# Optimization experiments

Hardware: AMD Instinct MI355X
Metric: run time of the kernel (lower is better)

The kernel has to match this reference:

```python
import jax, jax.numpy as jnp
import numpy as np

N, E = 50000, 800000
IN_DIM, HID, HEADS, OUT_DIM = 128, 64, 4, 64
NEG_SLOPE = 0.2


def add_self_loops(edge_index, n):
    loops = jnp.arange(n, dtype=edge_index.dtype)
    return jnp.concatenate([edge_index, jnp.stack([loops, loops])], axis=1)


def gat_layer(x, edge_index, W, att_src, att_dst, bias, heads, ch, concat):
    n = x.shape[0]
    xp = (x @ W).reshape(n, heads, ch)                       # [N,H,C]
    s_src = jnp.sum(xp * att_src, axis=-1)                   # [N,H]
    s_dst = jnp.sum(xp * att_dst, axis=-1)                   # [N,H]
    src, dst = edge_index[0], edge_index[1]
    e = jax.nn.leaky_relu(s_src[src] + s_dst[dst], NEG_SLOPE)  # [E,H]
    # segment softmax over incoming edges of each destination node
    m = jax.ops.segment_max(e, dst, num_segments=n)
    e = jnp.exp(e - m[dst])
    denom = jax.ops.segment_sum(e, dst, num_segments=n)
    alpha = e / (denom[dst] + 1e-16)                         # [E,H]
    out = jax.ops.segment_sum(xp[src] * alpha[:, :, None], dst, num_segments=n)  # [N,H,C]
    out = out.reshape(n, heads * ch) if concat else out.mean(axis=1)
    return out + bias


def setup_inputs() -> dict:
    key = jax.random.key(0)
    ks = jax.random.split(key, 10)
    glorot = lambda k, shape: jax.random.normal(k, shape, jnp.float32) * np.sqrt(2.0 / (shape[0] + shape[-1]))
    return {
        "x": jax.random.normal(ks[0], (N, IN_DIM), jnp.float32),
        "edge_index": jax.random.randint(ks[1], (2, E), 0, N, jnp.int32),
        "W1": glorot(ks[2], (IN_DIM, HEADS * HID)),
        "att_src1": glorot(ks[3], (HEADS, HID)),
        "att_dst1": glorot(ks[4], (HEADS, HID)),
        "bias1": jnp.zeros((HEADS * HID,), jnp.float32),
        "W2": glorot(ks[5], (HEADS * HID, OUT_DIM)),
        "att_src2": glorot(ks[6], (1, OUT_DIM)),
        "att_dst2": glorot(ks[7], (1, OUT_DIM)),
        "bias2": jnp.zeros((OUT_DIM,), jnp.float32),
    }


def reference(x, edge_index, W1, att_src1, att_dst1, bias1, W2, att_src2, att_dst2, bias2):
    ei = add_self_loops(edge_index, x.shape[0])
    h = gat_layer(x, ei, W1, att_src1, att_dst1, bias1, HEADS, HID, concat=True)
    h = jax.nn.relu(h)
    out = gat_layer(h, ei, W2, att_src2, att_dst2, bias2, 1, OUT_DIM, concat=False)
    return out
```

## Files before the change

### kernel.cpp

```cpp
#include <hip/hip_runtime.h>
#include <hip/hip_bf16.h>
#include <hip/hip_fp16.h>

#define NODES 50000
#define NEDGE 800000
#define NE2   850000
#define INDIM 128
#define F1    256
#define HEADS 4
#define HID   64
#define OUTD  64
#define MTILES 3125

#define NB   196
#define PB   196
#define EPB  4096
#define CAP  6144
#define G1B  782

typedef _Float16 f16;
typedef _Float16 f16x8 __attribute__((ext_vector_type(8)));
typedef float    f32x4 __attribute__((ext_vector_type(4)));

__global__ void k_hist(const int* __restrict__ ei, int* __restrict__ blkhist,
                       const float* __restrict__ W1, const float* __restrict__ W2,
                       f16* __restrict__ W1p, f16* __restrict__ W2p)
{
    const int b = blockIdx.x, t = threadIdx.x;
    if (b < PB) {
        __shared__ int h[NB];
        for (int i = t; i < NB; i += 256) h[i] = 0;
        __syncthreads();
        const int e0 = b * EPB;
        const int eend = min(e0 + EPB, NEDGE);
        for (int i = e0 + t; i < eend; i += 256) {
            int d = ei[NEDGE + i];
            atomicAdd(&h[d >> 8], 1);
        }
        __syncthreads();
        for (int i = t; i < NB; i += 256) blkhist[i * PB + b] = h[i];
    } else {
        int idx = (b - PB) * 256 + t;
        if (idx < 32768) {
            int j = idx & 7, l = (idx >> 3) & 63, fi = idx >> 9;
            int kb = fi & 3, ct = fi >> 2;
            int k = kb * 32 + (l >> 4) * 8 + j;
            int col = ct * 16 + (l & 15);
            W1p[idx] = (f16)W1[k * F1 + col];
        } else {
            int i2 = idx - 32768;
            int j = i2 & 7, l = (i2 >> 3) & 63, fi = i2 >> 9;
            int kb = fi & 7, ct = fi >> 3;
            int k = kb * 32 + (l >> 4) * 8 + j;
            int col = ct * 16 + (l & 15);
            W2p[i2] = (f16)W2[k * OUTD + col];
        }
    }
}

__global__ void k_scanR(int* __restrict__ blkhist, int* __restrict__ rowtot)
{
    __shared__ int sh[256];
    const int q = blockIdx.x, t = threadIdx.x;
    int v = (t < PB) ? blkhist[q * PB + t] : 0;
    sh[t] = v; __syncthreads();
    for (int off = 1; off < 256; off <<= 1) {
        int tv = (t >= off) ? sh[t - off] : 0;
        __syncthreads();
        sh[t] += tv;
        __syncthreads();
    }
    if (t < PB) blkhist[q * PB + t] = sh[t] - v;
    if (t == 255) rowtot[q] = sh[255];
}

__global__ void k_part(const int* __restrict__ ei, const int* __restrict__ blkhist,
                       const int* __restrict__ rowtot, unsigned* __restrict__ staged)
{
    const int b = blockIdx.x, t = threadIdx.x;
    __shared__ int sS[256];
    __shared__ int cur[NB];
    int v = (t < NB) ? rowtot[t] : 0;
    sS[t] = v; __syncthreads();
    for (int off = 1; off < 256; off <<= 1) {
        int tv = (t >= off) ? sS[t - off] : 0;
        __syncthreads();
        sS[t] += tv;
        __syncthreads();
    }
    if (t < NB) cur[t] = (sS[t] - v) + blkhist[t * PB + b];
    __syncthreads();
    const int e0 = b * EPB;
    const int eend = min(e0 + EPB, NEDGE);
    for (int i = e0 + t; i < eend; i += 256) {
        int sN = ei[i];
        int d  = ei[NEDGE + i];
        int pos = atomicAdd(&cur[d >> 8], 1);
        staged[pos] = (unsigned)sN | ((unsigned)(d & 255) << 16);
    }
}

__global__ __launch_bounds__(256) void k_bg(
    const unsigned* __restrict__ staged, const int* __restrict__ rowtot,
    int* __restrict__ row_ptr, int* __restrict__ csr_src,
    const float* __restrict__ x, const f16* __restrict__ W1p,
    const float* __restrict__ as1, const float* __restrict__ ad1,
    f16* __restrict__ xp1h, float* __restrict__ ssrc, float* __restrict__ sdst)
{
    if (blockIdx.x < NB) {
        __shared__ unsigned sorted2[CAP];
        __shared__ int bin[256];
        __shared__ int cnt[256];
        __shared__ int sh[256];
        __shared__ int ssum[4];
        const int q = blockIdx.x, t = threadIdx.x;
        const int wv = t >> 6, lane = t & 63;
        int pv = (t < q) ? rowtot[t] : 0;
#pragma unroll
        for (int off = 32; off; off >>= 1) pv += __shfl_xor(pv, off);
        if (lane == 0) ssum[wv] = pv;
        cnt[t] = 0; bin[t] = 0;
        __syncthreads();
        const int estart = ssum[0] + ssum[1] + ssum[2] + ssum[3];
        const int m = rowtot[q];
        const int nodebase = q * 256;
        const int nn = min(256, NODES - nodebase);
        const int csrbase = estart + nodebase;

        const bool dosort = (m <= CAP);
        if (dosort) {
            for (int i = t; i < m; i += 256)
                atomicAdd(&bin[(staged[estart + i] & 0xFFFFu) >> 8], 1);
            __syncthreads();
            int bv = bin[t];
            sh[t] = bv;
            __syncthreads();
            for (int off = 1; off < 256; off <<= 1) {
                int tv = (t >= off) ? sh[t - off] : 0;
                __syncthreads();
                sh[t] += tv;
                __syncthreads();
            }
            bin[t] = sh[t] - bv;
            __syncthreads();
            for (int i = t; i < m; i += 256) {
                unsigned u = staged[estart + i];
                int p = atomicAdd(&bin[(u & 0xFFFFu) >> 8], 1);
                sorted2[p] = u;
            }
            __syncthreads();
        }

        if (dosort) {
            for (int i = t; i < m; i += 256)
                atomicAdd(&cnt[sorted2[i] >> 16], 1);
        } else {
            for (int i = t; i < m; i += 256)
                atomicAdd(&cnt[staged[estart + i] >> 16], 1);
        }
        __syncthreads();
        int v = cnt[t];
        sh[t] = v;
        __syncthreads();
        for (int off = 1; off < 256; off <<= 1) {
            int tv = (t >= off) ? sh[t - off] : 0;
            __syncthreads();
            sh[t] += tv;
            __syncthreads();
        }
        int excl = sh[t] - v;
        __syncthreads();
        if (t < nn) {
            int r = csrbase + excl + t;
            row_ptr[nodebase + t] = r;
            csr_src[r] = nodebase + t;
            cnt[t] = excl + t + 1;
        }
        __syncthreads();
        if (dosort) {
            for (int i = t; i < m; i += 256) {
                unsigned u = sorted2[i];
                int pos = atomicAdd(&cnt[u >> 16], 1);
                csr_src[csrbase + pos] = (int)(u & 0xFFFFu);
            }
        } else {
            for (int i = t; i < m; i += 256) {
                unsigned u = staged[estart + i];
                int pos = atomicAdd(&cnt[u >> 16], 1);
                csr_src[csrbase + pos] = (int)(u & 0xFFFFu);
            }
        }
        if (q == NB - 1 && t == 0) row_ptr[NODES] = NE2;
        return;
    }

    const int wv = threadIdx.x >> 6, lane = threadIdx.x & 63;
    const int l15 = lane & 15, quad = lane >> 4;
    const int rowtile = (blockIdx.x - NB) * 4 + wv;
    if (rowtile >= MTILES) return;
    const int rowbase = rowtile * 16;

    f16x8 afrag[4];
    const float* xrow = x + (rowbase + l15) * INDIM + quad * 8;
#pragma unroll
    for (int kb = 0; kb < 4; ++kb) {
        float4 u0 = *(const float4*)(xrow + kb * 32);
        float4 u1 = *(const float4*)(xrow + kb * 32 + 4);
        f16x8 a;
        a[0] = (f16)u0.x; a[1] = (f16)u0.y; a[2] = (f16)u0.z; a[3] = (f16)u0.w;
        a[4] = (f16)u1.x; a[5] = (f16)u1.y; a[6] = (f16)u1.z; a[7] = (f16)u1.w;
        afrag[kb] = a;
    }

    const f16x8* Wf = (const f16x8*)W1p;
    f32x4 acc[16];
#pragma unroll
    for (int ct = 0; ct < 16; ++ct) acc[ct] = (f32x4){0.f, 0.f, 0.f, 0.f};
#pragma unroll
    for (int ct = 0; ct < 16; ++ct) {
#pragma unroll
        for (int kb = 0; kb < 4; ++kb) {
            f16x8 b = Wf[(ct * 4 + kb) * 64 + lane];
            acc[ct] = __builtin_amdgcn_mfma_f32_16x16x32_f16(afrag[kb], b, acc[ct], 0, 0, 0);
        }
    }
    const int orow = rowbase + quad * 4;
#pragma unroll
    for (int ct = 0; ct < 16; ++ct) {
#pragma unroll
        for (int r = 0; r < 4; ++r)
            xp1h[(orow + r) * F1 + ct * 16 + l15] = (f16)acc[ct][r];
    }
    float ps[4][4], pd[4][4];
#pragma unroll
    for (int h = 0; h < 4; ++h)
#pragma unroll
        for (int r = 0; r < 4; ++r) { ps[h][r] = 0.f; pd[h][r] = 0.f; }
#pragma unroll
    for (int ct = 0; ct < 16; ++ct) {
        float av = as1[ct * 16 + l15];
        float dv = ad1[ct * 16 + l15];
        int h = ct >> 2;
#pragma unroll
        for (int r = 0; r < 4; ++r) {
            ps[h][r] = fmaf(acc[ct][r], av, ps[h][r]);
            pd[h][r] = fmaf(acc[ct][r], dv, pd[h][r]);
        }
    }
#pragma unroll
    for (int off = 8; off; off >>= 1) {
#pragma unroll
        for (int h = 0; h < 4; ++h)
#pragma unroll
            for (int r = 0; r < 4; ++r) {
                ps[h][r] += __shfl_xor(ps[h][r], off);
                pd[h][r] += __shfl_xor(pd[h][r], off);
            }
    }
    if (l15 == 0) {
#pragma unroll
        for (int r = 0; r < 4; ++r) {
            int row = orow + r;
            float4 vs = {ps[0][r], ps[1][r], ps[2][r], ps[3][r]};
            float4 vd = {pd[0][r], pd[1][r], pd[2][r], pd[3][r]};
            ((float4*)ssrc)[row] = vs;
            ((float4*)sdst)[row] = vd;
        }
    }
}

__global__ __launch_bounds__(512) void k_agg1f(
    const int* __restrict__ row_ptr, const int* __restrict__ csr_src,
    const float* __restrict__ ssrc, const float* __restrict__ sdst,
    const f16* __restrict__ xp1h, const float* __restrict__ bias,
    const f16* __restrict__ W2p, const float* __restrict__ as2,
    const float* __restrict__ ad2,
    f16* __restrict__ xp2h, float* __restrict__ ssrc2, float* __restrict__ sdst2)
{
    __shared__ f16 hl[16][256];
    f16x8* hu = (f16x8*)&hl[0][0];
    const int t = threadIdx.x;
    if (t < 256) hu[256 + t] = (f16x8){0,0,0,0,0,0,0,0};

    const int wv = t >> 6, l = t & 63;
    const int n = blockIdx.x * 8 + wv;
    const int eq = l & 15, ph = l >> 4;
    const int g  = l >> 4, sub = l & 15;
    const int sel_lo = (sub >> 3) << 4;
    const int sel_hi = (2 + (sub >> 3)) << 4;
    const float sd = sdst[n * HEADS + ph];
    const int jbeg = row_ptr[n], jend = row_ptr[n + 1];
    const f16x8* xv = (const f16x8*)xp1h;

    float den = 0.f;
    float alo[8] = {0.f,0.f,0.f,0.f,0.f,0.f,0.f,0.f};
    float ahi[8] = {0.f,0.f,0.f,0.f,0.f,0.f,0.f,0.f};
    for (int base = jbeg; base < jend; base += 16) {
        int c = jend - base; if (c > 16) c = 16;
        int s = 0; float ex = 0.f;
        if (eq < c) {
            s = csr_src[base + eq];
            float e = ssrc[s * HEADS + ph] + sd;
            e = e > 0.f ? e : 0.2f * e;
            ex = __expf(e);
        }
        den += ex;
        int p = 0;
        for (; p + 7 < c; p += 8) {
            int ea = p + g, eb = p + 4 + g;
            int   sa  = __shfl(s, ea),          sb  = __shfl(s, eb);
            float aal = __shfl(ex, ea | sel_lo), aah = __shfl(ex, ea | sel_hi);
            float abl = __shfl(ex, eb | sel_lo), abh = __shfl(ex, eb | sel_hi);
            f16x8 va0 = xv[sa * 32 + sub];
            f16x8 va1 = xv[sa * 32 + sub + 16];
            f16x8 vb0 = xv[sb * 32 + sub];
            f16x8 vb1 = xv[sb * 32 + sub + 16];
#pragma unroll
            for (int j = 0; j < 8; ++j) {
                alo[j] = fmaf(aal, (float)va0[j], alo[j]);
                ahi[j] = fmaf(aah, (float)va1[j], ahi[j]);
            }
#pragma unroll
            for (int j = 0; j < 8; ++j) {
                alo[j] = fmaf(abl, (float)vb0[j], alo[j]);
                ahi[j] = fmaf(abh, (float)vb1[j], ahi[j]);
            }
        }
        for (; p < c; p += 4) {
            int ea = p + g;
            int   sa  = __shfl(s, ea);
            float aal = __shfl(ex, ea | sel_lo), aah = __shfl(ex, ea | sel_hi);
            f16x8 va0 = xv[sa * 32 + sub];
            f16x8 va1 = xv[sa * 32 + sub + 16];
#pragma unroll
            for (int j = 0; j < 8; ++j) {
                alo[j] = fmaf(aal, (float)va0[j], alo[j]);
                ahi[j] = fmaf(aah, (float)va1[j], ahi[j]);
            }
        }
    }
#pragma unroll
    for (int off = 8; off; off >>= 1) den += __shfl_xor(den, off);
    const float dl = __shfl(den, sel_lo);
    const float dh = __shfl(den, sel_hi);
    const float rdl = 1.f / (dl + 1e-16f);
    const float rdh = 1.f / (dh + 1e-16f);
#pragma unroll
    for (int j = 0; j < 8; ++j) {
        alo[j] += __shfl_xor(alo[j], 16); alo[j] += __shfl_xor(alo[j], 32);
        ahi[j] += __shfl_xor(ahi[j], 16); ahi[j] += __shfl_xor(ahi[j], 32);
    }
    if (g == 0) {
        const float4* b4 = (const float4*)bias;
        float4 bl0 = b4[sub * 2],        bl1 = b4[sub * 2 + 1];
        float4 bh0 = b4[(sub + 16) * 2], bh1 = b4[(sub + 16) * 2 + 1];
        f16x8 olo, ohi;
        float v;
        v = fmaf(alo[0], rdl, bl0.x); olo[0] = (f16)(v > 0.f ? v : 0.f);
        v = fmaf(alo[1], rdl, bl0.y); olo[1] = (f16)(v > 0.f ? v : 0.f);
        v = fmaf(alo[2], rdl, bl0.z); olo[2] = (f16)(v > 0.f ? v : 0.f);
        v = fmaf(alo[3], rdl, bl0.w); olo[3] = (f16)(v > 0.f ? v : 0.f);
        v = fmaf(alo[4], rdl, bl1.x); olo[4] = (f16)(v > 0.f ? v : 0.f);
        v = fmaf(alo[5], rdl, bl1.y); olo[5] = (f16)(v > 0.f ? v : 0.f);
        v = fmaf(alo[6], rdl, bl1.z); olo[6] = (f16)(v > 0.f ? v : 0.f);
        v = fmaf(alo[7], rdl, bl1.w); olo[7] = (f16)(v > 0.f ? v : 0.f);
        v = fmaf(ahi[0], rdh, bh0.x); ohi[0] = (f16)(v > 0.f ? v : 0.f);
        v = fmaf(ahi[1], rdh, bh0.y); ohi[1] = (f16)(v > 0.f ? v : 0.f);
        v = fmaf(ahi[2], rdh, bh0.z); ohi[2] = (f16)(v > 0.f ? v : 0.f);
        v = fmaf(ahi[3], rdh, bh0.w); ohi[3] = (f16)(v > 0.f ? v : 0.f);
        v = fmaf(ahi[4], rdh, bh1.x); ohi[4] = (f16)(v > 0.f ? v : 0.f);
        v = fmaf(ahi[5], rdh, bh1.y); ohi[5] = (f16)(v > 0.f ? v : 0.f);
        v = fmaf(ahi[6], rdh, bh1.z); ohi[6] = (f16)(v > 0.f ? v : 0.f);
        v = fmaf(ahi[7], rdh, bh1.w); ohi[7] = (f16)(v > 0.f ? v : 0.f);
        hu[wv * 32 + sub]      = olo;
        hu[wv * 32 + sub + 16] = ohi;
    }
    __syncthreads();

    if (wv == 0) {
        const int lane = l;
        const int l15 = lane & 15, quad = lane >> 4;
        const f16x8* Wf = (const f16x8*)W2p;
        f32x4 acc2[4];
#pragma unroll
        for (int ct = 0; ct < 4; ++ct) acc2[ct] = (f32x4){0.f, 0.f, 0.f, 0.f};
#pragma unroll
        for (int kb = 0; kb < 8; ++kb) {
            f16x8 a = hu[l15 * 32 + quad + kb * 4];
#pragma unroll
            for (int ct = 0; ct < 4; ++ct) {
                f16x8 b = Wf[(ct * 8 + kb) * 64 + lane];
                acc2[ct] = __builtin_amdgcn_mfma_f32_16x16x32_f16(a, b, acc2[ct], 0, 0, 0);
            }
        }
        const int rowbase = blockIdx.x * 8;
#pragma unroll
        for (int ct = 0; ct < 4; ++ct) {
#pragma unroll
            for (int r = 0; r < 4; ++r) {
                int row = quad * 4 + r;
                if (row < 8)
                    xp2h[(rowbase + row) * OUTD + ct * 16 + l15] = (f16)acc2[ct][r];
            }
        }
        float ps[4] = {0.f,0.f,0.f,0.f}, pd[4] = {0.f,0.f,0.f,0.f};
#pragma unroll
        for (int ct = 0; ct < 4; ++ct) {
            float av = as2[ct * 16 + l15];
            float dv = ad2[ct * 16 + l15];
#pragma unroll
            for (int r = 0; r < 4; ++r) {
                ps[r] = fmaf(acc2[ct][r], av, ps[r]);
                pd[r] = fmaf(acc2[ct][r], dv, pd[r]);
            }
        }
#pragma unroll
        for (int off = 8; off; off >>= 1) {
#pragma unroll
            for (int r = 0; r < 4; ++r) {
                ps[r] += __shfl_xor(ps[r], off);
                pd[r] += __shfl_xor(pd[r], off);
            }
        }
        if (l15 == 0) {
#pragma unroll
            for (int r = 0; r < 4; ++r) {
                int row = quad * 4 + r;
                if (row < 8) {
                    ssrc2[rowbase + row] = ps[r];
                    sdst2[rowbase + row] = pd[r];
                }
            }
        }
    }
}

__global__ __launch_bounds__(256) void k_agg2(
    const int* __restrict__ row_ptr, const int* __restrict__ csr_src,
    const float* __restrict__ ssrc, const float* __restrict__ sdst,
    const f16* __restrict__ xp2h, const float* __restrict__ bias,
    float* __restrict__ out)
{
    const int wv = threadIdx.x >> 6, l = threadIdx.x & 63;
    const int n = blockIdx.x * 4 + wv;
    const int grp = l >> 3, sub = l & 7;
    const float sd = sdst[n];
    const int jbeg = row_ptr[n], jend = row_ptr[n + 1];
    const f16x8* xv = (const f16x8*)xp2h;

    float den = 0.f;
    float acc[8] = {0.f,0.f,0.f,0.f,0.f,0.f,0.f,0.f};
    for (int base = jbeg; base < jend; base += 64) {
        int c = jend - base; if (c > 64) c = 64;
        int s = 0; float ex = 0.f;
        if (l < c) {
            s = csr_src[base + l];
            float e = ssrc[s] + sd;
            e = e > 0.f ? e : 0.2f * e;
            ex = __expf(e);
        }
        den += ex;
        int i = 0;
        for (; 8 * (i + 1) < c; i += 2) {
            int ea = 8 * i + grp, eb = 8 * i + 8 + grp;
            int   sa = __shfl(s, ea),  sb = __shfl(s, eb);
            float aa = __shfl(ex, ea), ab = __shfl(ex, eb);
            f16x8 va = xv[sa * 8 + sub];
            f16x8 vb = xv[sb * 8 + sub];
#pragma unroll
            for (int j = 0; j < 8; ++j) acc[j] = fmaf(aa, (float)va[j], acc[j]);
#pragma unroll
            for (int j = 0; j < 8; ++j) acc[j] = fmaf(ab, (float)vb[j], acc[j]);
        }
        for (; 8 * i < c; ++i) {
            int eidx = 8 * i + grp;
            int   se = __shfl(s, eidx);
            float ae = __shfl(ex, eidx);
            f16x8 v = xv[se * 8 + sub];
#pragma unroll
            for (int j = 0; j < 8; ++j) acc[j] = fmaf(ae, (float)v[j], acc[j]);
        }
    }
#pragma unroll
    for (int off = 32; off; off >>= 1) den += __shfl_xor(den, off);
    const float rd = 1.f / (den + 1e-16f);
#pragma unroll
    for (int j = 0; j < 8; ++j) {
        acc[j] += __shfl_xor(acc[j], 8);
        acc[j] += __shfl_xor(acc[j], 16);
        acc[j] += __shfl_xor(acc[j], 32);
    }
    if (grp == 0) {
        const float4* b4 = (const float4*)bias;
        float4 ba = b4[sub * 2], bb = b4[sub * 2 + 1];
        float4 o0, o1;
        o0.x = fmaf(acc[0], rd, ba.x); o0.y = fmaf(acc[1], rd, ba.y);
        o0.z = fmaf(acc[2], rd, ba.z); o0.w = fmaf(acc[3], rd, ba.w);
        o1.x = fmaf(acc[4], rd, bb.x); o1.y = fmaf(acc[5], rd, bb.y);
        o1.z = fmaf(acc[6], rd, bb.z); o1.w = fmaf(acc[7], rd, bb.w);
        float4* ov = (float4*)out + n * 16 + sub * 2;
        ov[0] = o0; ov[1] = o1;
    }
}

extern "C" void kernel_launch(void* const* d_in, const int* in_sizes, int n_in,
                              void* d_out, int out_size, void* d_ws, size_t ws_size,
                              hipStream_t stream)
{
    (void)in_sizes; (void)n_in; (void)out_size; (void)ws_size;
    const float* x   = (const float*)d_in[0];
    const int*   ei  = (const int*)d_in[1];
    const float* W1  = (const float*)d_in[2];
    const float* as1 = (const float*)d_in[3];
    const float* ad1 = (const float*)d_in[4];
    const float* b1  = (const float*)d_in[5];
    const float* W2  = (const float*)d_in[6];
    const float* as2 = (const float*)d_in[7];
    const float* ad2 = (const float*)d_in[8];
    const float* b2  = (const float*)d_in[9];
    float* out = (float*)d_out;

    f16* xp1h    = (f16*)d_ws;
    f16* xp2h    = xp1h + (size_t)NODES * F1;
    f16* W1p     = xp2h + (size_t)NODES * OUTD;
    f16* W2p     = W1p + 32768;
    float* ssrc1 = (float*)(W2p + 16384);
    float* sdst1 = ssrc1 + (size_t)NODES * HEADS;
    float* ssrc2 = sdst1 + (size_t)NODES * HEADS;
    float* sdst2 = ssrc2 + (size_t)NODES;
    int* row_ptr = (int*)(sdst2 + (size_t)NODES);
    int* blkhist = row_ptr + NODES + 1;
    int* rowtot  = blkhist + NB * PB;
    int* csr_src = rowtot + NB;
    unsigned* staged = (unsigned*)(csr_src + NE2);

    k_hist<<<PB + 192, 256, 0, stream>>>(ei, blkhist, W1, W2, W1p, W2p);
    k_scanR<<<NB, 256, 0, stream>>>(blkhist, rowtot);
    k_part<<<PB, 256, 0, stream>>>(ei, blkhist, rowtot, staged);

    k_bg<<<NB + G1B, 256, 0, stream>>>(staged, rowtot, row_ptr, csr_src,
                                       x, W1p, as1, ad1, xp1h, ssrc1, sdst1);

    k_agg1f<<<NODES / 8, 512, 0, stream>>>(row_ptr, csr_src, ssrc1, sdst1,
                                           xp1h, b1, W2p, as2, ad2,
                                           xp2h, ssrc2, sdst2);

    k_agg2<<<NODES / 4, 256, 0, stream>>>(row_ptr, csr_src, ssrc2, sdst2,
                                          xp2h, b2, out);
}
```

Measured before the change: 227.4 us.

## Fuse bucket scan into partition kernel and fill MFMA tile with 16 nodes

```diff
diff --git a/kernel.cpp b/kernel.cpp
--- a/kernel.cpp
+++ b/kernel.cpp
@@ -17,6 +17,8 @@
 #define EPB  4096
 #define CAP  6144
 #define G1B  782
+
+#define LP   264
 
 typedef _Float16 f16;
 typedef _Float16 f16x8 __attribute__((ext_vector_type(8)));
@@ -58,37 +60,31 @@
     }
 }
 
-__global__ void k_scanR(int* __restrict__ blkhist, int* __restrict__ rowtot)
-{
-    __shared__ int sh[256];
-    const int q = blockIdx.x, t = threadIdx.x;
-    int v = (t < PB) ? blkhist[q * PB + t] : 0;
-    sh[t] = v; __syncthreads();
-    for (int off = 1; off < 256; off <<= 1) {
-        int tv = (t >= off) ? sh[t - off] : 0;
-        __syncthreads();
-        sh[t] += tv;
-        __syncthreads();
-    }
-    if (t < PB) blkhist[q * PB + t] = sh[t] - v;
-    if (t == 255) rowtot[q] = sh[255];
-}
-
 __global__ void k_part(const int* __restrict__ ei, const int* __restrict__ blkhist,
-                       const int* __restrict__ rowtot, unsigned* __restrict__ staged)
+                       int* __restrict__ rowtot, unsigned* __restrict__ staged)
 {
     const int b = blockIdx.x, t = threadIdx.x;
     __shared__ int sS[256];
     __shared__ int cur[NB];
-    int v = (t < NB) ? rowtot[t] : 0;
-    sS[t] = v; __syncthreads();
+    int rowsum = 0, colpref = 0;
+    if (t < NB) {
+        const int* hrow = blkhist + t * PB;
+        for (int p = 0; p < PB; ++p) {
+            int h = hrow[p];
+            colpref += (p < b) ? h : 0;
+            rowsum += h;
+        }
+        if (b == 0) rowtot[t] = rowsum;
+    }
+    sS[t] = (t < NB) ? rowsum : 0;
+    __syncthreads();
     for (int off = 1; off < 256; off <<= 1) {
         int tv = (t >= off) ? sS[t - off] : 0;
         __syncthreads();
         sS[t] += tv;
         __syncthreads();
     }
-    if (t < NB) cur[t] = (sS[t] - v) + blkhist[t * PB + b];
+    if (t < NB) cur[t] = (sS[t] - rowsum) + colpref;
     __syncthreads();
     const int e0 = b * EPB;
     const int eend = min(e0 + EPB, NEDGE);
@@ -269,7 +265,7 @@
     }
 }
 
-__global__ __launch_bounds__(512) void k_agg1f(
+__global__ __launch_bounds__(512) void k_agg1g(
     const int* __restrict__ row_ptr, const int* __restrict__ csr_src,
     const float* __restrict__ ssrc, const float* __restrict__ sdst,
     const f16* __restrict__ xp1h, const float* __restrict__ bias,
@@ -277,103 +273,108 @@
     const float* __restrict__ ad2,
     f16* __restrict__ xp2h, float* __restrict__ ssrc2, float* __restrict__ sdst2)
 {
-    __shared__ f16 hl[16][256];
-    f16x8* hu = (f16x8*)&hl[0][0];
+    __shared__ f16 hl[16][LP];
     const int t = threadIdx.x;
-    if (t < 256) hu[256 + t] = (f16x8){0,0,0,0,0,0,0,0};
-
     const int wv = t >> 6, l = t & 63;
-    const int n = blockIdx.x * 8 + wv;
     const int eq = l & 15, ph = l >> 4;
     const int g  = l >> 4, sub = l & 15;
     const int sel_lo = (sub >> 3) << 4;
     const int sel_hi = (2 + (sub >> 3)) << 4;
-    const float sd = sdst[n * HEADS + ph];
-    const int jbeg = row_ptr[n], jend = row_ptr[n + 1];
     const f16x8* xv = (const f16x8*)xp1h;
-
-    float den = 0.f;
-    float alo[8] = {0.f,0.f,0.f,0.f,0.f,0.f,0.f,0.f};
-    float ahi[8] = {0.f,0.f,0.f,0.f,0.f,0.f,0.f,0.f};
-    for (int base = jbeg; base < jend; base += 16) {
-        int c = jend - base; if (c > 16) c = 16;
-        int s = 0; float ex = 0.f;
-        if (eq < c) {
-            s = csr_src[base + eq];
-            float e = ssrc[s * HEADS + ph] + sd;
-            e = e > 0.f ? e : 0.2f * e;
-            ex = __expf(e);
-        }
-        den += ex;
-        int p = 0;
-        for (; p + 7 < c; p += 8) {
-            int ea = p + g, eb = p + 4 + g;
-            int   sa  = __shfl(s, ea),          sb  = __shfl(s, eb);
-            float aal = __shfl(ex, ea | sel_lo), aah = __shfl(ex, ea | sel_hi);
-            float abl = __shfl(ex, eb | sel_lo), abh = __shfl(ex, eb | sel_hi);
-            f16x8 va0 = xv[sa * 32 + sub];
-            f16x8 va1 = xv[sa * 32 + sub + 16];
-            f16x8 vb0 = xv[sb * 32 + sub];
-            f16x8 vb1 = xv[sb * 32 + sub + 16];
-#pragma unroll
-            for (int j = 0; j < 8; ++j) {
-                alo[j] = fmaf(aal, (float)va0[j], alo[j]);
-                ahi[j] = fmaf(aah, (float)va1[j], ahi[j]);
-            }
-#pragma unroll
-            for (int j = 0; j < 8; ++j) {
-                alo[j] = fmaf(abl, (float)vb0[j], alo[j]);
-                ahi[j] = fmaf(abh, (float)vb1[j], ahi[j]);
-            }
-        }
-        for (; p < c; p += 4) {
-            int ea = p + g;
-            int   sa  = __shfl(s, ea);
-            float aal = __shfl(ex, ea | sel_lo), aah = __shfl(ex, ea | sel_hi);
-            f16x8 va0 = xv[sa * 32 + sub];
-            f16x8 va1 = xv[sa * 32 + sub + 16];
-#pragma unroll
-            for (int j = 0; j < 8; ++j) {
-                alo[j] = fmaf(aal, (float)va0[j], alo[j]);
-                ahi[j] = fmaf(aah, (float)va1[j], ahi[j]);
-            }
-        }
-    }
-#pragma unroll
-    for (int off = 8; off; off >>= 1) den += __shfl_xor(den, off);
-    const float dl = __shfl(den, sel_lo);
-    const float dh = __shfl(den, sel_hi);
-    const float rdl = 1.f / (dl + 1e-16f);
-    const float rdh = 1.f / (dh + 1e-16f);
-#pragma unroll
-    for (int j = 0; j < 8; ++j) {
-        alo[j] += __shfl_xor(alo[j], 16); alo[j] += __shfl_xor(alo[j], 32);
-        ahi[j] += __shfl_xor(ahi[j], 16); ahi[j] += __shfl_xor(ahi[j], 32);
-    }
-    if (g == 0) {
-        const float4* b4 = (const float4*)bias;
-        float4 bl0 = b4[sub * 2],        bl1 = b4[sub * 2 + 1];
-        float4 bh0 = b4[(sub + 16) * 2], bh1 = b4[(sub + 16) * 2 + 1];
-        f16x8 olo, ohi;
-        float v;
-        v = fmaf(alo[0], rdl, bl0.x); olo[0] = (f16)(v > 0.f ? v : 0.f);
-        v = fmaf(alo[1], rdl, bl0.y); olo[1] = (f16)(v > 0.f ? v : 0.f);
-        v = fmaf(alo[2], rdl, bl0.z); olo[2] = (f16)(v > 0.f ? v : 0.f);
-        v = fmaf(alo[3], rdl, bl0.w); olo[3] = (f16)(v > 0.f ? v : 0.f);
-        v = fmaf(alo[4], rdl, bl1.x); olo[4] = (f16)(v > 0.f ? v : 0.f);
-        v = fmaf(alo[5], rdl, bl1.y); olo[5] = (f16)(v > 0.f ? v : 0.f);
-        v = fmaf(alo[6], rdl, bl1.z); olo[6] = (f16)(v > 0.f ? v : 0.f);
-        v = fmaf(alo[7], rdl, bl1.w); olo[7] = (f16)(v > 0.f ? v : 0.f);
-        v = fmaf(ahi[0], rdh, bh0.x); ohi[0] = (f16)(v > 0.f ? v : 0.f);
-        v = fmaf(ahi[1], rdh, bh0.y); ohi[1] = (f16)(v > 0.f ? v : 0.f);
-        v = fmaf(ahi[2], rdh, bh0.z); ohi[2] = (f16)(v > 0.f ? v : 0.f);
-        v = fmaf(ahi[3], rdh, bh0.w); ohi[3] = (f16)(v > 0.f ? v : 0.f);
-        v = fmaf(ahi[4], rdh, bh1.x); ohi[4] = (f16)(v > 0.f ? v : 0.f);
-        v = fmaf(ahi[5], rdh, bh1.y); ohi[5] = (f16)(v > 0.f ? v : 0.f);
-        v = fmaf(ahi[6], rdh, bh1.z); ohi[6] = (f16)(v > 0.f ? v : 0.f);
-        v = fmaf(ahi[7], rdh, bh1.w); ohi[7] = (f16)(v > 0.f ? v : 0.f);
-        hu[wv * 32 + sub]      = olo;
-        hu[wv * 32 + sub + 16] = ohi;
+    const int nodebase = blockIdx.x * 16;
+
+#pragma unroll
+    for (int pass = 0; pass < 2; ++pass) {
+        const int row = wv + pass * 8;
+        const int n = nodebase + row;
+        const float sd = sdst[n * HEADS + ph];
+        const int jbeg = row_ptr[n], jend = row_ptr[n + 1];
+
+        float den = 0.f;
+        float alo[8] = {0.f,0.f,0.f,0.f,0.f,0.f,0.f,0.f};
+        float ahi[8] = {0.f,0.f,0.f,0.f,0.f,0.f,0.f,0.f};
+        for (int base = jbeg; base < jend; base += 16) {
+            int c = jend - base; if (c > 16) c = 16;
+            int s = 0; float ex = 0.f;
+            if (eq < c) {
+                s = csr_src[base + eq];
+                float e = ssrc[s * HEADS + ph] + sd;
+                e = e > 0.f ? e : 0.2f * e;
+                ex = __expf(e);
+            }
+            den += ex;
+            int p = 0;
+            for (; p + 7 < c; p += 8) {
+                int ea = p + g, eb = p + 4 + g;
+                int   sa  = __shfl(s, ea),          sb  = __shfl(s, eb);
+                float aal = __shfl(ex, ea | sel_lo), aah = __shfl(ex, ea | sel_hi);
+                float abl = __shfl(ex, eb | sel_lo), abh = __shfl(ex, eb | sel_hi);
+                f16x8 va0 = xv[sa * 32 + sub];
+                f16x8 va1 = xv[sa * 32 + sub + 16];
+                f16x8 vb0 = xv[sb * 32 + sub];
+                f16x8 vb1 = xv[sb * 32 + sub + 16];
+#pragma unroll
+                for (int j = 0; j < 8; ++j) {
+                    alo[j] = fmaf(aal, (float)va0[j], alo[j]);
+                    ahi[j] = fmaf(aah, (float)va1[j], ahi[j]);
+                }
+#pragma unroll
+                for (int j = 0; j < 8; ++j) {
+                    alo[j] = fmaf(abl, (float)vb0[j], alo[j]);
+                    ahi[j] = fmaf(abh, (float)vb1[j], ahi[j]);
+                }
+            }
+            for (; p < c; p += 4) {
+                int ea = p + g;
+                int   sa  = __shfl(s, ea);
+                float aal = __shfl(ex, ea | sel_lo), aah = __shfl(ex, ea | sel_hi);
+                f16x8 va0 = xv[sa * 32 + sub];
+                f16x8 va1 = xv[sa * 32 + sub + 16];
+#pragma unroll
+                for (int j = 0; j < 8; ++j) {
+                    alo[j] = fmaf(aal, (float)va0[j], alo[j]);
+                    ahi[j] = fmaf(aah, (float)va1[j], ahi[j]);
+                }
+            }
+        }
+#pragma unroll
+        for (int off = 8; off; off >>= 1) den += __shfl_xor(den, off);
+        const float dl = __shfl(den, sel_lo);
+        const float dh = __shfl(den, sel_hi);
+        const float rdl = 1.f / (dl + 1e-16f);
+        const float rdh = 1.f / (dh + 1e-16f);
+#pragma unroll
+        for (int j = 0; j < 8; ++j) {
+            alo[j] += __shfl_xor(alo[j], 16); alo[j] += __shfl_xor(alo[j], 32);
+            ahi[j] += __shfl_xor(ahi[j], 16); ahi[j] += __shfl_xor(ahi[j], 32);
+        }
+        if (g == 0) {
+            const float4* b4 = (const float4*)bias;
+            float4 bl0 = b4[sub * 2],        bl1 = b4[sub * 2 + 1];
+            float4 bh0 = b4[(sub + 16) * 2], bh1 = b4[(sub + 16) * 2 + 1];
+            f16x8 olo, ohi;
+            float v;
+            v = fmaf(alo[0], rdl, bl0.x); olo[0] = (f16)(v > 0.f ? v : 0.f);
+            v = fmaf(alo[1], rdl, bl0.y); olo[1] = (f16)(v > 0.f ? v : 0.f);
+            v = fmaf(alo[2], rdl, bl0.z); olo[2] = (f16)(v > 0.f ? v : 0.f);
+            v = fmaf(alo[3], rdl, bl0.w); olo[3] = (f16)(v > 0.f ? v : 0.f);
+            v = fmaf(alo[4], rdl, bl1.x); olo[4] = (f16)(v > 0.f ? v : 0.f);
+            v = fmaf(alo[5], rdl, bl1.y); olo[5] = (f16)(v > 0.f ? v : 0.f);
+            v = fmaf(alo[6], rdl, bl1.z); olo[6] = (f16)(v > 0.f ? v : 0.f);
+            v = fmaf(alo[7], rdl, bl1.w); olo[7] = (f16)(v > 0.f ? v : 0.f);
+            v = fmaf(ahi[0], rdh, bh0.x); ohi[0] = (f16)(v > 0.f ? v : 0.f);
+            v = fmaf(ahi[1], rdh, bh0.y); ohi[1] = (f16)(v > 0.f ? v : 0.f);
+            v = fmaf(ahi[2], rdh, bh0.z); ohi[2] = (f16)(v > 0.f ? v : 0.f);
+            v = fmaf(ahi[3], rdh, bh0.w); ohi[3] = (f16)(v > 0.f ? v : 0.f);
+            v = fmaf(ahi[4], rdh, bh1.x); ohi[4] = (f16)(v > 0.f ? v : 0.f);
+            v = fmaf(ahi[5], rdh, bh1.y); ohi[5] = (f16)(v > 0.f ? v : 0.f);
+            v = fmaf(ahi[6], rdh, bh1.z); ohi[6] = (f16)(v > 0.f ? v : 0.f);
+            v = fmaf(ahi[7], rdh, bh1.w); ohi[7] = (f16)(v > 0.f ? v : 0.f);
+            *(f16x8*)&hl[row][sub * 8]       = olo;
+            *(f16x8*)&hl[row][128 + sub * 8] = ohi;
+        }
+#pragma unroll
+        for (int j = 0; j < 8; ++j) { alo[j] = 0.f; ahi[j] = 0.f; }
     }
     __syncthreads();
 
@@ -386,22 +387,18 @@
         for (int ct = 0; ct < 4; ++ct) acc2[ct] = (f32x4){0.f, 0.f, 0.f, 0.f};
 #pragma unroll
         for (int kb = 0; kb < 8; ++kb) {
-            f16x8 a = hu[l15 * 32 + quad + kb * 4];
+            f16x8 a = *(const f16x8*)&hl[l15][quad * 8 + kb * 32];
 #pragma unroll
             for (int ct = 0; ct < 4; ++ct) {
                 f16x8 b = Wf[(ct * 8 + kb) * 64 + lane];
                 acc2[ct] = __builtin_amdgcn_mfma_f32_16x16x32_f16(a, b, acc2[ct], 0, 0, 0);
             }
         }
-        const int rowbase = blockIdx.x * 8;
 #pragma unroll
         for (int ct = 0; ct < 4; ++ct) {
 #pragma unroll
-            for (int r = 0; r < 4; ++r) {
-                int row = quad * 4 + r;
-                if (row < 8)
-                    xp2h[(rowbase + row) * OUTD + ct * 16 + l15] = (f16)acc2[ct][r];
-            }
+            for (int r = 0; r < 4; ++r)
+                xp2h[(nodebase + quad * 4 + r) * OUTD + ct * 16 + l15] = (f16)acc2[ct][r];
         }
         float ps[4] = {0.f,0.f,0.f,0.f}, pd[4] = {0.f,0.f,0.f,0.f};
 #pragma unroll
@@ -425,11 +422,8 @@
         if (l15 == 0) {
 #pragma unroll
             for (int r = 0; r < 4; ++r) {
-                int row = quad * 4 + r;
-                if (row < 8) {
-                    ssrc2[rowbase + row] = ps[r];
-                    sdst2[rowbase + row] = pd[r];
-                }
+                ssrc2[nodebase + quad * 4 + r] = ps[r];
+                sdst2[nodebase + quad * 4 + r] = pd[r];
             }
         }
     }
@@ -535,15 +529,14 @@
     unsigned* staged = (unsigned*)(csr_src + NE2);
 
     k_hist<<<PB + 192, 256, 0, stream>>>(ei, blkhist, W1, W2, W1p, W2p);
-    k_scanR<<<NB, 256, 0, stream>>>(blkhist, rowtot);
     k_part<<<PB, 256, 0, stream>>>(ei, blkhist, rowtot, staged);
 
     k_bg<<<NB + G1B, 256, 0, stream>>>(staged, rowtot, row_ptr, csr_src,
                                        x, W1p, as1, ad1, xp1h, ssrc1, sdst1);
 
-    k_agg1f<<<NODES / 8, 512, 0, stream>>>(row_ptr, csr_src, ssrc1, sdst1,
-                                           xp1h, b1, W2p, as2, ad2,
-                                           xp2h, ssrc2, sdst2);
+    k_agg1g<<<NODES / 16, 512, 0, stream>>>(row_ptr, csr_src, ssrc1, sdst1,
+                                            xp1h, b1, W2p, as2, ad2,
+                                            xp2h, ssrc2, sdst2);
 
     k_agg2<<<NODES / 4, 256, 0, stream>>>(row_ptr, csr_src, ssrc2, sdst2,
                                           xp2h, b2, out);
```

New measurement: 233.9 us. +2.9%, slower.
